# Optimization experiments

Measured on AMD Instinct MI355X. Metric: run time of the kernel, lower is better.

The kernel has to match this reference:

```python
import jax, jax.numpy as jnp
import numpy as np

N_NODES = 100000
N_EDGES = 500000
N_GRAPHS = 128
HID = 128          # Config.hidden_dim
KEY_EMB = HID // 4 # 32
IN_DIM = 16
FEAT_DIM = IN_DIM - 1  # key feature removed
OUT_DIM = 2
MSG_IN = 2 * HID + 1   # 257


def setup_inputs() -> dict:
    key = jax.random.key(0)
    ks = jax.random.split(key, 24)
    p = lambda k, shp: (jax.random.normal(k, shp, dtype=jnp.float32) * 0.02)
    inp = {
        "x": jax.random.normal(ks[0], (N_NODES, IN_DIM), dtype=jnp.float32),
        "W_enc": p(ks[1], (1, KEY_EMB)), "b_enc": jnp.zeros((KEY_EMB,), jnp.float32),
        "W0": p(ks[2], (FEAT_DIM + KEY_EMB, HID)), "b0": jnp.zeros((HID,), jnp.float32),
        "W1a": p(ks[3], (MSG_IN, HID)), "b1a": jnp.zeros((HID,), jnp.float32),
        "W1b": p(ks[4], (HID, HID)), "b1b": jnp.zeros((HID,), jnp.float32),
        "W2a": p(ks[5], (MSG_IN, HID)), "b2a": jnp.zeros((HID,), jnp.float32),
        "W2b": p(ks[6], (HID, HID)), "b2b": jnp.zeros((HID,), jnp.float32),
        "Wf1": p(ks[7], (4 * HID, HID)), "bf1": jnp.zeros((HID,), jnp.float32),
        "Wf2": p(ks[8], (HID, OUT_DIM)), "bf2": jnp.zeros((OUT_DIM,), jnp.float32),
        "edge_src1": jax.random.randint(ks[9], (N_EDGES,), 0, N_NODES),
        "edge_dst1": jax.random.randint(ks[10], (N_EDGES,), 0, N_NODES),
        "edge_src2": jax.random.randint(ks[11], (N_EDGES,), 0, N_NODES),
        "edge_dst2": jax.random.randint(ks[12], (N_EDGES,), 0, N_NODES),
        "batch": jnp.sort(jax.random.randint(ks[13], (N_NODES,), 0, N_GRAPHS)),
    }
    return inp


def _leaky_relu(v):
    return jnp.where(v > 0, v, 0.1 * v)


def _edge_conv(h, key_feat, src, dst, Wa, ba, Wb, bb):
    # message: [x_j - x_i, x_i, key_j - key_i] -> Linear -> LeakyReLU(0.1) -> Linear
    h_i = h[dst]                      # [E, HID] target
    h_j = h[src]                      # [E, HID] source
    m = jnp.concatenate([h_j - h_i, h_i, key_feat[src] - key_feat[dst]], axis=-1)  # [E, 257]
    m = _leaky_relu(jnp.dot(m, Wa) + ba)
    m = jnp.dot(m, Wb) + bb
    agg = jax.ops.segment_max(m, dst, num_segments=N_NODES)
    agg = jnp.where(jnp.isfinite(agg), agg, 0.0)  # nodes with no in-edges -> 0 (PyG scatter-max fill)
    return agg + h  # residual


def reference(x, W_enc, b_enc, W0, b0, W1a, b1a, W1b, b1b, W2a, b2a, W2b, b2b,
              Wf1, bf1, Wf2, bf2, edge_src1, edge_dst1, edge_src2, edge_dst2, batch):
    key_feat = x[:, 0:1]              # key_feature_idx = 0
    features = x[:, 1:]               # [N, FEAT_DIM]
    key_emb = jnp.dot(key_feat, W_enc) + b_enc  # [N, 32]
    h = jax.nn.relu(jnp.dot(jnp.concatenate([features, key_emb], axis=-1), W0) + b0)  # dropout: eval mode

    x1 = jax.nn.relu(_edge_conv(h, key_feat, edge_src1, edge_dst1, W1a, b1a, W1b, b1b))
    x2 = jax.nn.relu(_edge_conv(x1, key_feat, edge_src2, edge_dst2, W2a, b2a, W2b, b2b))

    cat = jnp.concatenate([x1, x2], axis=1)  # [N, 256]
    max_pool = jax.ops.segment_max(cat, batch, num_segments=N_GRAPHS)
    max_pool = jnp.where(jnp.isfinite(max_pool), max_pool, 0.0)
    counts = jax.ops.segment_sum(jnp.ones((N_NODES,), jnp.float32), batch, num_segments=N_GRAPHS)
    mean_pool = jax.ops.segment_sum(cat, batch, num_segments=N_GRAPHS) / jnp.maximum(counts, 1.0)[:, None]

    pooled = jnp.concatenate([max_pool, mean_pool], axis=1)  # [G, 512]
    out = jnp.dot(jax.nn.relu(jnp.dot(pooled, Wf1) + bf1), Wf2) + bf2
    return jax.nn.log_softmax(out, axis=1)
```

## Files before the change

### kernel.cpp

```cpp
#include <hip/hip_runtime.h>
#include <cstdint>

#define N_NODES 100000
#define N_EDGES 500000
#define N_GRAPHS 128
#define HID 128
#define SCAN1_B ((2 * N_NODES + 255) / 256)
#define BOTH_GRID ((2 * N_EDGES + 255) / 256)

typedef __attribute__((ext_vector_type(8))) short short8;
typedef __attribute__((ext_vector_type(4))) float f32x4;

__device__ __forceinline__ unsigned encf(float f) {
    unsigned u = __float_as_uint(f);
    return (u & 0x80000000u) ? ~u : (u | 0x80000000u);
}
__device__ __forceinline__ float decf(unsigned e) {
    unsigned u = (e & 0x80000000u) ? (e & 0x7FFFFFFFu) : ~e;
    return __uint_as_float(u);
}
__device__ __forceinline__ unsigned pk_bf16(float a, float b) {
    unsigned ua = __float_as_uint(a);
    unsigned ub = __float_as_uint(b);
    ua = (ua + 0x7fffu + ((ua >> 16) & 1u)) >> 16;
    ub = (ub + 0x7fffu + ((ub >> 16) & 1u)) & 0xffff0000u;
    return ua | ub;
}
__device__ __forceinline__ ushort bf16r(float f) {
    unsigned u = __float_as_uint(f);
    return (ushort)((u + 0x7fffu + ((u >> 16) & 1u)) >> 16);
}
__device__ __forceinline__ float bf2f(ushort h) {
    return __uint_as_float((unsigned)h << 16);
}

__global__ __launch_bounds__(256) void transp_prep_kernel(const float* __restrict__ W1b,
                                                          const float* __restrict__ W2b,
                                                          const float* __restrict__ W1a,
                                                          const float* __restrict__ W2a,
                                                          const float* __restrict__ W_enc,
                                                          const float* __restrict__ b_enc,
                                                          const float* __restrict__ W0,
                                                          const float* __restrict__ b0,
                                                          ushort* __restrict__ WT,
                                                          float* __restrict__ wkey,
                                                          float* __restrict__ bias0,
                                                          int* __restrict__ cnt,
                                                          float* __restrict__ pooled) {
    int blk = blockIdx.x;
    int tid = threadIdx.x;
    if (blk >= 385) {
        int z = blk - 385;
        if (z < SCAN1_B) {
            int i = z * 256 + tid;
            if (i < 2 * N_NODES) cnt[i] = 0;
        } else {
            int i = (z - SCAN1_B) * 256 + tid;
            pooled[i] = 0.f;
        }
        return;
    }
    if (blk == 384) {
        if (tid < HID) {
            float wk = 0.f, bk = b0[tid];
            for (int k = 0; k < 32; ++k) {
                float w = W0[(15 + k) * HID + tid];
                wk += W_enc[k] * w;
                bk += b_enc[k] * w;
            }
            wkey[tid] = wk;
            bias0[tid] = bk;
        }
        return;
    }
    int m = blk >> 6;
    int i = (blk & 63) * 256 + tid;
    int n = i >> 7, k = i & 127;
    int src = k * HID + n;
    float v;
    switch (m) {
        case 0: v = W1b[src]; break;
        case 1: v = W2b[src]; break;
        case 2: v = W1a[src]; break;
        case 3: v = W1a[HID * HID + src] - W1a[src]; break;
        case 4: v = W2a[src]; break;
        default: v = W2a[HID * HID + src] - W2a[src]; break;
    }
    WT[m * HID * HID + i] = bf16r(v);
}

__global__ __launch_bounds__(256) void encode_hist_kernel(const float* __restrict__ x,
                                                          const float* __restrict__ W0,
                                                          const float* __restrict__ wkey,
                                                          const float* __restrict__ bias0,
                                                          ushort* __restrict__ h,
                                                          float* __restrict__ xkey,
                                                          const int* __restrict__ dst1,
                                                          const int* __restrict__ dst2,
                                                          int* __restrict__ cnt,
                                                          int* __restrict__ seq) {
    int blk = blockIdx.x;
    int tid = threadIdx.x;
    if (blk < BOTH_GRID) {
        int e = blk * 256 + tid;
        if (e < N_EDGES) seq[e] = atomicAdd(&cnt[dst1[e]], 1);
        else if (e < 2 * N_EDGES) seq[e] = atomicAdd(&cnt[N_NODES + dst2[e - N_EDGES]], 1);
        return;
    }
    int nb = blk - BOTH_GRID;
    int n = nb * 2 + (tid >> 7);
    int j = tid & 127;
    const float* xr = x + n * 16;
    float k0 = xr[0];
    if (j == 0) xkey[n] = k0;
    float acc = bias0[j] + k0 * wkey[j];
#pragma unroll
    for (int f = 0; f < 15; ++f)
        acc = fmaf(xr[1 + f], W0[f * HID + j], acc);
    h[n * HID + j] = bf16r(fmaxf(acc, 0.f));
}

__global__ __launch_bounds__(512, 4) void mm_mfma_dual_kernel(const ushort* __restrict__ in,
                                                              const unsigned* __restrict__ aggin,
                                                              const int* __restrict__ cntin,
                                                              const float* __restrict__ baddin,
                                                              ushort* __restrict__ xout,
                                                              const ushort* __restrict__ WuT,
                                                              const ushort* __restrict__ WvT,
                                                              const float* __restrict__ bv,
                                                              ushort* __restrict__ outu,
                                                              ushort* __restrict__ outv, int nrows) {
    __shared__ ushort sH[128 * 136];
    __shared__ ushort sWT[128 * 136];
    int tid = threadIdx.x;
    int n0 = blockIdx.x * 128;
#pragma unroll
    for (int q = 0; q < 4; ++q) {
        int c = q * 512 + tid;
        int r = c >> 4, off = (c & 15) << 3;
        int n = n0 + r;
        uint4 vv = make_uint4(0, 0, 0, 0);
        if (n < nrows) {
            uint4 hv = *(const uint4*)(in + (size_t)n * HID + off);
            if (aggin) {
                float add[8];
#pragma unroll
                for (int p = 0; p < 8; ++p) add[p] = 0.f;
                if (cntin[n] > 0) {
                    uint4 e0 = *(const uint4*)(aggin + (size_t)n * HID + off);
                    uint4 e1 = *(const uint4*)(aggin + (size_t)n * HID + off + 4);
                    float4 bb0 = *(const float4*)(baddin + off);
                    float4 bb1 = *(const float4*)(baddin + off + 4);
                    add[0] = decf(e0.x) + bb0.x; add[1] = decf(e0.y) + bb0.y;
                    add[2] = decf(e0.z) + bb0.z; add[3] = decf(e0.w) + bb0.w;
                    add[4] = decf(e1.x) + bb1.x; add[5] = decf(e1.y) + bb1.y;
                    add[6] = decf(e1.z) + bb1.z; add[7] = decf(e1.w) + bb1.w;
                }
                unsigned hw[4] = {hv.x, hv.y, hv.z, hv.w};
                unsigned ow[4];
#pragma unroll
                for (int p = 0; p < 4; ++p) {
                    float lo = __uint_as_float(hw[p] << 16);
                    float hi = __uint_as_float(hw[p] & 0xffff0000u);
                    float r0 = fmaxf(add[2 * p] + lo, 0.f);
                    float r1 = fmaxf(add[2 * p + 1] + hi, 0.f);
                    ow[p] = pk_bf16(r0, r1);
                }
                vv = make_uint4(ow[0], ow[1], ow[2], ow[3]);
                *(uint4*)(xout + (size_t)n * HID + off) = vv;
            } else {
                vv = hv;
            }
        }
        *(uint4*)(sH + r * 136 + off) = vv;
    }
#pragma unroll
    for (int q = 0; q < 4; ++q) {
        int c = q * 512 + tid;
        int nn = c >> 4, off = (c & 15) << 3;
        *(uint4*)(sWT + nn * 136 + off) = *(const uint4*)(WuT + nn * 128 + off);
    }
    __syncthreads();

    int lane = tid & 63, wv = tid >> 6;
    int l15 = lane & 15, quad = lane >> 4;
    int ch = wv & 1, rh = wv >> 1;

    short8 afr[2][4];
#pragma unroll
    for (int rr = 0; rr < 2; ++rr) {
        const ushort* ab = sH + (rh * 32 + rr * 16 + l15) * 136 + quad * 8;
#pragma unroll
        for (int kc = 0; kc < 4; ++kc)
            afr[rr][kc] = *(const short8*)(ab + kc * 32);
    }

#pragma unroll
    for (int pass = 0; pass < 2; ++pass) {
        ushort* out = pass ? outv : outu;
        f32x4 acc[2][4];
#pragma unroll
        for (int rr = 0; rr < 2; ++rr)
#pragma unroll
            for (int ct = 0; ct < 4; ++ct) acc[rr][ct] = (f32x4){0.f, 0.f, 0.f, 0.f};
#pragma unroll
        for (int kc = 0; kc < 4; ++kc) {
#pragma unroll
            for (int ct = 0; ct < 4; ++ct) {
                short8 bfr = *(const short8*)(sWT + ((ch * 4 + ct) * 16 + l15) * 136 + quad * 8 + kc * 32);
                acc[0][ct] = __builtin_amdgcn_mfma_f32_16x16x32_bf16(afr[0][kc], bfr, acc[0][ct], 0, 0, 0);
                acc[1][ct] = __builtin_amdgcn_mfma_f32_16x16x32_bf16(afr[1][kc], bfr, acc[1][ct], 0, 0, 0);
            }
        }
        __syncthreads();
#pragma unroll
        for (int ct = 0; ct < 4; ++ct) {
            int col = (ch * 4 + ct) * 16 + l15;
            float bb = pass ? bv[col] : 0.f;
#pragma unroll
            for (int rr = 0; rr < 2; ++rr) {
                int rowb = rh * 32 + rr * 16 + quad * 4;
#pragma unroll
                for (int reg = 0; reg < 4; ++reg)
                    sH[(rowb + reg) * 136 + col] = bf16r(acc[rr][ct][reg] + bb);
            }
        }
        if (pass == 0) {
#pragma unroll
            for (int q = 0; q < 4; ++q) {
                int c = q * 512 + tid;
                int nn = c >> 4, off = (c & 15) << 3;
                *(uint4*)(sWT + nn * 136 + off) = *(const uint4*)(WvT + nn * 128 + off);
            }
        }
        __syncthreads();
#pragma unroll
        for (int q = 0; q < 4; ++q) {
            int c = q * 512 + tid;
            int r = c >> 4, off = (c & 15) << 3;
            int m = n0 + r;
            if (m < nrows)
                *(uint4*)(out + (size_t)m * HID + off) = *(const uint4*)(sH + r * 136 + off);
        }
    }
}

__global__ __launch_bounds__(256) void scan1_kernel(const int* __restrict__ cnt,
                                                    int* __restrict__ cursor,
                                                    int* __restrict__ partials) {
    __shared__ int tmp[256];
    int tid = threadIdx.x;
    int gid = blockIdx.x * 256 + tid;
    int v = (gid < 2 * N_NODES) ? cnt[gid] : 0;
    tmp[tid] = v;
    __syncthreads();
#pragma unroll
    for (int off = 1; off < 256; off <<= 1) {
        int t = (tid >= off) ? tmp[tid - off] : 0;
        __syncthreads();
        tmp[tid] += t;
        __syncthreads();
    }
    if (gid < 2 * N_NODES) cursor[gid] = tmp[tid] - v;
    if (tid == 255) partials[blockIdx.x] = tmp[255];
}

__global__ __launch_bounds__(1024) void scan2_kernel(int* __restrict__ partials) {
    __shared__ int tmp[1024];
    int tid = threadIdx.x;
    int v = (tid < SCAN1_B) ? partials[tid] : 0;
    tmp[tid] = v;
    __syncthreads();
#pragma unroll
    for (int off = 1; off < 1024; off <<= 1) {
        int t = (tid >= off) ? tmp[tid - off] : 0;
        __syncthreads();
        tmp[tid] += t;
        __syncthreads();
    }
    if (tid < SCAN1_B) partials[tid] = tmp[tid] - v;
}

__global__ __launch_bounds__(256) void build_kernel(const int* __restrict__ src1,
                                                    const int* __restrict__ dst1,
                                                    const int* __restrict__ src2,
                                                    const int* __restrict__ dst2,
                                                    const int* __restrict__ cnt,
                                                    const int* __restrict__ cursor,
                                                    const int* __restrict__ partials,
                                                    const int* __restrict__ seq,
                                                    int* __restrict__ srcS,
                                                    int* __restrict__ dstS,
                                                    unsigned* __restrict__ agg1,
                                                    unsigned* __restrict__ agg2) {
    int blk = blockIdx.x;
    int tid = threadIdx.x;
    if (blk < SCAN1_B) {
        int gid = blk * 256 + tid;
        if (gid >= 2 * N_NODES) return;
        int c = cnt[gid];
        if (c == 0) return;
        int o = cursor[gid] + partials[gid >> 8];
        int layer = gid >= N_NODES;
        int d = gid - layer * N_NODES;
        for (int i = 0; i < c; ++i) dstS[o + i] = d;
        bool spans = (o >> 4) != ((o + c - 1) >> 4);
        bool tail = (o + c == N_EDGES) || (o + c == 2 * N_EDGES);
        if (spans || tail) {
            unsigned* agg = layer ? agg2 : agg1;
            uint4* ap = (uint4*)(agg + (size_t)d * HID);
#pragma unroll
            for (int i = 0; i < 32; ++i) ap[i] = make_uint4(0u, 0u, 0u, 0u);
        }
        return;
    }
    int e = (blk - SCAN1_B) * 256 + tid;
    int s, idx;
    if (e < N_EDGES) { s = src1[e]; idx = dst1[e]; }
    else if (e < 2 * N_EDGES) { s = src2[e - N_EDGES]; idx = N_NODES + dst2[e - N_EDGES]; }
    else return;
    int pos = cursor[idx] + partials[idx >> 8] + seq[e];
    srcS[pos] = s;
}

__global__ __launch_bounds__(512, 6) void edge_kernel(const ushort* __restrict__ u,
                                                      const ushort* __restrict__ v,
                                                      const float* __restrict__ xkey,
                                                      const int* __restrict__ srcS,
                                                      const int* __restrict__ dstS,
                                                      const ushort* __restrict__ WbT,
                                                      const float* __restrict__ wlast,
                                                      unsigned* __restrict__ agg) {
    __shared__ ushort sWT[128 * 136];
    __shared__ ushort sU[64 * 136];
    __shared__ int sDst[64];
    __shared__ int sBnd[2];
    __shared__ unsigned sMask[3];
    int tid = threadIdx.x;
    int w0 = blockIdx.x * 64;

#pragma unroll
    for (int q = 0; q < 4; ++q) {
        int c = q * 512 + tid;
        int n = c >> 4, off = (c & 15) << 3;
        *(uint4*)(sWT + n * 136 + off) = *(const uint4*)(WbT + n * 128 + off);
    }

    int eloc = tid >> 3;
    int sub = tid & 7;
    int kb = sub << 4;
    int lane = tid & 63, wv = tid >> 6;
    int l15 = lane & 15, quad = lane >> 4;
    int ch = wv & 1, rh = wv >> 1;

    float wreg[16];
    {
        const float4* wr4 = (const float4*)(wlast + kb);
#pragma unroll
        for (int q = 0; q < 4; ++q) {
            float4 wq = wr4[q];
            wreg[q * 4 + 0] = wq.x; wreg[q * 4 + 1] = wq.y;
            wreg[q * 4 + 2] = wq.z; wreg[q * 4 + 3] = wq.w;
        }
    }

    {
        int e = w0 + eloc;
        if (e >= N_EDGES) e = N_EDGES - 1;
        int sx = srcS[e], sy = dstS[e];
        if (sub == 0) sDst[eloc] = sy;
        if (tid < 2) {
            int eb = (tid == 0) ? (w0 - 1) : (w0 + 64);
            sBnd[tid] = (eb >= 0 && eb < N_EDGES) ? dstS[eb] : -1;
        }
        float kd = xkey[sx] - xkey[sy];
        const uint4* ur = (const uint4*)(u + (size_t)sx * HID + kb);
        const uint4* vr = (const uint4*)(v + (size_t)sy * HID + kb);
        uint4 uu[2], vvv[2];
        uu[0] = ur[0]; uu[1] = ur[1];
        vvv[0] = vr[0]; vvv[1] = vr[1];
#pragma unroll
        for (int q = 0; q < 2; ++q) {
            unsigned pu[4] = {uu[q].x, uu[q].y, uu[q].z, uu[q].w};
            unsigned pv[4] = {vvv[q].x, vvv[q].y, vvv[q].z, vvv[q].w};
            unsigned pk[4];
#pragma unroll
            for (int p = 0; p < 4; ++p) {
                float a0 = __uint_as_float(pu[p] << 16) + __uint_as_float(pv[p] << 16);
                float a1 = __uint_as_float(pu[p] & 0xffff0000u) + __uint_as_float(pv[p] & 0xffff0000u);
                a0 = fmaf(kd, wreg[q * 8 + 2 * p], a0);
                a1 = fmaf(kd, wreg[q * 8 + 2 * p + 1], a1);
                a0 = fmaxf(a0, 0.1f * a0);
                a1 = fmaxf(a1, 0.1f * a1);
                pk[p] = pk_bf16(a0, a1);
            }
            uint4 o; o.x = pk[0]; o.y = pk[1]; o.z = pk[2]; o.w = pk[3];
            *(uint4*)(sU + eloc * 136 + kb + q * 8) = o;
        }
    }
    __syncthreads();

    if (tid < 64) {
        int dprev = (tid == 0) ? sBnd[0] : sDst[tid - 1];
        unsigned long long m = __ballot(sDst[tid] != dprev);
        if (tid == 0) { sMask[0] = (unsigned)m; sMask[1] = (unsigned)(m >> 32); }
        if (tid == 63) sMask[2] = (sDst[63] != sBnd[1]) ? 1u : 0u;
    }

    short8 afr[4];
    {
        const ushort* ab = sU + (rh * 16 + l15) * 136 + quad * 8;
#pragma unroll
        for (int kc = 0; kc < 4; ++kc)
            afr[kc] = *(const short8*)(ab + kc * 32);
    }
    f32x4 acc[4];
#pragma unroll
    for (int ct = 0; ct < 4; ++ct) acc[ct] = (f32x4){0.f, 0.f, 0.f, 0.f};
#pragma unroll
    for (int kc = 0; kc < 4; ++kc) {
#pragma unroll
        for (int ct = 0; ct < 4; ++ct) {
            short8 bfr = *(const short8*)(sWT + ((ch * 4 + ct) * 16 + l15) * 136 + quad * 8 + kc * 32);
            acc[ct] = __builtin_amdgcn_mfma_f32_16x16x32_bf16(afr[kc], bfr, acc[ct], 0, 0, 0);
        }
    }
    __syncthreads();

#pragma unroll
    for (int ct = 0; ct < 4; ++ct) {
        int col = (ch * 4 + ct) * 16 + l15;
        uint2 pr;
        pr.x = pk_bf16(acc[ct][0], acc[ct][1]);
        pr.y = pk_bf16(acc[ct][2], acc[ct][3]);
        *(uint2*)(sU + col * 66 + rh * 16 + quad * 4) = pr;
    }
    __syncthreads();

    {
        int j = tid & 127;
        int q4 = tid >> 7;
        int base = q4 * 16;
        const ushort* mrow = sU + j * 66 + base;
        float vals[16];
#pragma unroll
        for (int q = 0; q < 4; ++q) {
            ushort4 mv = *(const ushort4*)(mrow + q * 4);
            vals[q * 4 + 0] = bf2f(mv.x);
            vals[q * 4 + 1] = bf2f(mv.y);
            vals[q * 4 + 2] = bf2f(mv.z);
            vals[q * 4 + 3] = bf2f(mv.w);
        }
        unsigned mlo = __builtin_amdgcn_readfirstlane(sMask[0]);
        unsigned mhi = __builtin_amdgcn_readfirstlane(sMask[1]);
        unsigned b64 = __builtin_amdgcn_readfirstlane(sMask[2]);
        unsigned long long mask = ((unsigned long long)mhi << 32) | mlo;
        unsigned slice = (unsigned)((mask >> base) & 0xFFFFull);
        unsigned nextbit = (q4 == 3) ? (b64 & 1u) : (unsigned)((mask >> (base + 16)) & 1ull);
        unsigned ext = slice | (nextbit << 16);
        bool contFrom = !(ext & 1u);
        float run = 0.f;
        bool first = true;
#pragma unroll
        for (int e3 = 0; e3 < 16; ++e3) {
            float vv2 = vals[e3];
            bool hb = (ext >> e3) & 1u;
            run = (e3 == 0 || hb) ? vv2 : fmaxf(run, vv2);
            bool end = (e3 == 15) || ((ext >> (e3 + 1)) & 1u);
            if (end) {
                int d = sDst[base + e3];
                unsigned en = encf(run);
                unsigned* ap = agg + (size_t)d * HID + j;
                bool useAtomic = (first && contFrom) || ((e3 == 15) && !nextbit);
                if (useAtomic) atomicMax(ap, en);
                else *ap = en;
                first = false;
            }
        }
    }
}

__global__ __launch_bounds__(256) void pool_kernel(const ushort* __restrict__ x1,
                                                   const unsigned* __restrict__ agg2,
                                                   const float* __restrict__ b2b,
                                                   const int* __restrict__ cnt2,
                                                   const int* __restrict__ batch,
                                                   float* __restrict__ pooled) {
    int g = blockIdx.x >> 4, s = blockIdx.x & 15;
    int tid = threadIdx.x;
    int lo = 0, hi = N_NODES;
    while (lo < hi) { int mid = (lo + hi) >> 1; if (batch[mid] < g) lo = mid + 1; else hi = mid; }
    int start = lo;
    hi = N_NODES;
    while (lo < hi) { int mid = (lo + hi) >> 1; if (batch[mid] < g + 1) lo = mid + 1; else hi = mid; }
    int end = lo;
    int cnt = end - start;
    int b0 = start + (int)((long long)cnt * s / 16);
    int b1 = start + (int)((long long)cnt * (s + 1) / 16);
    if (b1 <= b0) return;
    int j = tid & 127;
    bool isx2 = tid >= 128;
    float bbj = isx2 ? b2b[j] : 0.f;
    float mx = -INFINITY, sm = 0.f;
    for (int n = b0; n < b1; ++n) {
        float xv = bf2f(x1[(size_t)n * HID + j]);
        float vv;
        if (isx2) {
            float a = 0.f;
            if (cnt2[n] > 0) a = decf(agg2[(size_t)n * HID + j]) + bbj;
            vv = fmaxf(a + xv, 0.f);
        } else {
            vv = xv;
        }
        mx = fmaxf(mx, vv);
        sm += vv;
    }
    atomicMax((unsigned*)pooled + (size_t)g * 512 + tid, encf(mx));
    atomicAdd(pooled + (size_t)g * 512 + 256 + tid, sm);
}

__global__ __launch_bounds__(128) void final_kernel(const float* __restrict__ pooled,
                                                    const int* __restrict__ batch,
                                                    const float* __restrict__ Wf1,
                                                    const float* __restrict__ bf1,
                                                    const float* __restrict__ Wf2,
                                                    const float* __restrict__ bf2,
                                                    float* __restrict__ out) {
    __shared__ float sP[512];
    __shared__ float sH[128];
    int g = blockIdx.x, tid = threadIdx.x;
    int lo = 0, hi = N_NODES;
    while (lo < hi) { int mid = (lo + hi) >> 1; if (batch[mid] < g) lo = mid + 1; else hi = mid; }
    int start = lo;
    hi = N_NODES;
    while (lo < hi) { int mid = (lo + hi) >> 1; if (batch[mid] < g + 1) lo = mid + 1; else hi = mid; }
    int cnt = lo - start;
    float inv = 1.f / (float)(cnt > 1 ? cnt : 1);
#pragma unroll
    for (int q = 0; q < 4; ++q) {
        int idx = q * 128 + tid;
        float raw;
        if (idx < 256) {
            unsigned e = ((const unsigned*)pooled)[(size_t)g * 512 + idx];
            raw = (e == 0u) ? 0.f : decf(e);
        } else {
            raw = pooled[(size_t)g * 512 + idx] * inv;
        }
        sP[idx] = raw;
    }
    __syncthreads();
    float acc = bf1[tid];
    for (int k = 0; k < 512; ++k) acc = fmaf(sP[k], Wf1[k * HID + tid], acc);
    sH[tid] = fmaxf(acc, 0.f);
    __syncthreads();
    if (tid < 2) {
        float l = bf2[tid];
        for (int k = 0; k < 128; ++k) l = fmaf(sH[k], Wf2[k * 2 + tid], l);
        sP[tid] = l;
    }
    __syncthreads();
    if (tid == 0) {
        float l0 = sP[0], l1 = sP[1];
        float m = fmaxf(l0, l1);
        float ls = m + logf(expf(l0 - m) + expf(l1 - m));
        out[g * 2 + 0] = l0 - ls;
        out[g * 2 + 1] = l1 - ls;
    }
}

extern "C" void kernel_launch(void* const* d_in, const int* in_sizes, int n_in,
                              void* d_out, int out_size, void* d_ws, size_t ws_size,
                              hipStream_t stream) {
    const float* x     = (const float*)d_in[0];
    const float* W_enc = (const float*)d_in[1];
    const float* b_enc = (const float*)d_in[2];
    const float* W0    = (const float*)d_in[3];
    const float* b0    = (const float*)d_in[4];
    const float* W1a   = (const float*)d_in[5];
    const float* b1a   = (const float*)d_in[6];
    const float* W1b   = (const float*)d_in[7];
    const float* b1b   = (const float*)d_in[8];
    const float* W2a   = (const float*)d_in[9];
    const float* b2a   = (const float*)d_in[10];
    const float* W2b   = (const float*)d_in[11];
    const float* b2b   = (const float*)d_in[12];
    const float* Wf1   = (const float*)d_in[13];
    const float* bf1   = (const float*)d_in[14];
    const float* Wf2   = (const float*)d_in[15];
    const float* bf2   = (const float*)d_in[16];
    const int* src1    = (const int*)d_in[17];
    const int* dst1    = (const int*)d_in[18];
    const int* src2    = (const int*)d_in[19];
    const int* dst2    = (const int*)d_in[20];
    const int* batch   = (const int*)d_in[21];

    const size_t NB = (size_t)N_NODES * HID;
    ushort* hbuf  = (ushort*)d_ws;
    unsigned* agg1 = (unsigned*)(hbuf + NB);
    unsigned* agg2 = agg1 + NB;
    ushort* ubuf  = (ushort*)(agg2 + NB);
    ushort* vbuf  = ubuf + NB;
    ushort* WT    = vbuf + NB;
    ushort* WbT1 = WT;
    ushort* WbT2 = WT + 1 * HID * HID;
    ushort* WuT1 = WT + 2 * HID * HID;
    ushort* WvT1 = WT + 3 * HID * HID;
    ushort* WuT2 = WT + 4 * HID * HID;
    ushort* WvT2 = WT + 5 * HID * HID;
    float* wkey  = (float*)(WT + 6 * HID * HID);
    float* bias0 = wkey + 128;
    float* xkey  = bias0 + 128;
    float* pooled = xkey + N_NODES;
    int* cnt    = (int*)(pooled + 128 * 512);
    int* cursor = cnt + 2 * N_NODES;
    int* partials = cursor + 2 * N_NODES;
    int* srcS = partials + 1024;
    int* dstS = srcS + 2 * N_EDGES;
    int* seq  = dstS + 2 * N_EDGES;

    const int edgeGrid = (N_EDGES + 63) / 64;
    const int mmGrid   = (N_NODES + 127) / 128;
    const int prepGrid = 385 + SCAN1_B + 256;
    const int encHistGrid = BOTH_GRID + N_NODES / 2;
    const int buildGrid = SCAN1_B + BOTH_GRID;

    transp_prep_kernel<<<prepGrid, 256, 0, stream>>>(W1b, W2b, W1a, W2a, W_enc, b_enc, W0, b0,
                                                     WT, wkey, bias0, cnt, pooled);
    encode_hist_kernel<<<encHistGrid, 256, 0, stream>>>(x, W0, wkey, bias0, hbuf, xkey,
                                                        dst1, dst2, cnt, seq);

    scan1_kernel<<<SCAN1_B, 256, 0, stream>>>(cnt, cursor, partials);
    scan2_kernel<<<1, 1024, 0, stream>>>(partials);
    build_kernel<<<buildGrid, 256, 0, stream>>>(src1, dst1, src2, dst2, cnt, cursor, partials,
                                                seq, srcS, dstS, agg1, agg2);

    mm_mfma_dual_kernel<<<mmGrid, 512, 0, stream>>>(hbuf, nullptr, nullptr, nullptr, nullptr,
                                                    WuT1, WvT1, b1a, ubuf, vbuf, N_NODES);
    edge_kernel<<<edgeGrid, 512, 0, stream>>>(ubuf, vbuf, xkey, srcS, dstS, WbT1,
                                              W1a + 256 * HID, agg1);

    mm_mfma_dual_kernel<<<mmGrid, 512, 0, stream>>>(hbuf, agg1, cnt, b1b, hbuf,
                                                    WuT2, WvT2, b2a, ubuf, vbuf, N_NODES);
    edge_kernel<<<edgeGrid, 512, 0, stream>>>(ubuf, vbuf, xkey, srcS + N_EDGES, dstS + N_EDGES,
                                              WbT2, W2a + 256 * HID, agg2);

    pool_kernel<<<N_GRAPHS * 16, 256, 0, stream>>>(hbuf, agg2, b2b, cnt + N_NODES, batch, pooled);
    final_kernel<<<N_GRAPHS, 128, 0, stream>>>(pooled, batch, Wf1, bf1, Wf2, bf2, (float*)d_out);
}
```

Measured before the change: 492.5 us.

## Fuse node encoding into first matmul and merge CSR build with it

The node encoder (x·W0 + key embedding, ReLU) now runs inside the first MFMA dual-matmul kernel. That kernel also carries the CSR build work (dst fill, agg zeroing, src scatter) as extra blocks, and the histogram moves into the prep kernel. The cnt buffer is zeroed with hipMemsetAsync instead of kernel blocks. This removes two launches and a round trip of h through memory before the first matmul, at the cost of a larger heterogeneous kernel whose build blocks share occupancy limits with the MFMA blocks.

New measurement: 463.3 us. 5.9% less time.

```diff
diff --git a/kernel.cpp b/kernel.cpp
--- a/kernel.cpp
+++ b/kernel.cpp
@@ -7,6 +7,9 @@
 #define HID 128
 #define SCAN1_B ((2 * N_NODES + 255) / 256)
 #define BOTH_GRID ((2 * N_EDGES + 255) / 256)
+#define MM_G ((N_NODES + 127) / 128)
+#define A_G ((2 * N_NODES + 511) / 512)
+#define B_G ((2 * N_EDGES + 511) / 512)
 
 typedef __attribute__((ext_vector_type(8))) short short8;
 typedef __attribute__((ext_vector_type(4))) float f32x4;
@@ -34,30 +37,32 @@
     return __uint_as_float((unsigned)h << 16);
 }
 
-__global__ __launch_bounds__(256) void transp_prep_kernel(const float* __restrict__ W1b,
-                                                          const float* __restrict__ W2b,
-                                                          const float* __restrict__ W1a,
-                                                          const float* __restrict__ W2a,
-                                                          const float* __restrict__ W_enc,
-                                                          const float* __restrict__ b_enc,
-                                                          const float* __restrict__ W0,
-                                                          const float* __restrict__ b0,
-                                                          ushort* __restrict__ WT,
-                                                          float* __restrict__ wkey,
-                                                          float* __restrict__ bias0,
-                                                          int* __restrict__ cnt,
-                                                          float* __restrict__ pooled) {
+__global__ __launch_bounds__(256) void prep_hist_kernel(const float* __restrict__ W1b,
+                                                        const float* __restrict__ W2b,
+                                                        const float* __restrict__ W1a,
+                                                        const float* __restrict__ W2a,
+                                                        const float* __restrict__ W_enc,
+                                                        const float* __restrict__ b_enc,
+                                                        const float* __restrict__ W0,
+                                                        const float* __restrict__ b0,
+                                                        ushort* __restrict__ WT,
+                                                        float* __restrict__ wkey,
+                                                        float* __restrict__ bias0,
+                                                        float* __restrict__ pooled,
+                                                        const int* __restrict__ dst1,
+                                                        const int* __restrict__ dst2,
+                                                        int* __restrict__ cnt,
+                                                        int* __restrict__ seq) {
     int blk = blockIdx.x;
     int tid = threadIdx.x;
+    if (blk >= 641) {
+        int e = (blk - 641) * 256 + tid;
+        if (e < N_EDGES) seq[e] = atomicAdd(&cnt[dst1[e]], 1);
+        else if (e < 2 * N_EDGES) seq[e] = atomicAdd(&cnt[N_NODES + dst2[e - N_EDGES]], 1);
+        return;
+    }
     if (blk >= 385) {
-        int z = blk - 385;
-        if (z < SCAN1_B) {
-            int i = z * 256 + tid;
-            if (i < 2 * N_NODES) cnt[i] = 0;
-        } else {
-            int i = (z - SCAN1_B) * 256 + tid;
-            pooled[i] = 0.f;
-        }
+        pooled[(blk - 385) * 256 + tid] = 0.f;
         return;
     }
     if (blk == 384) {
@@ -89,35 +94,203 @@
     WT[m * HID * HID + i] = bf16r(v);
 }
 
-__global__ __launch_bounds__(256) void encode_hist_kernel(const float* __restrict__ x,
+__global__ __launch_bounds__(256) void scan1_kernel(const int* __restrict__ cnt,
+                                                    int* __restrict__ cursor,
+                                                    int* __restrict__ partials) {
+    __shared__ int tmp[256];
+    int tid = threadIdx.x;
+    int gid = blockIdx.x * 256 + tid;
+    int v = (gid < 2 * N_NODES) ? cnt[gid] : 0;
+    tmp[tid] = v;
+    __syncthreads();
+#pragma unroll
+    for (int off = 1; off < 256; off <<= 1) {
+        int t = (tid >= off) ? tmp[tid - off] : 0;
+        __syncthreads();
+        tmp[tid] += t;
+        __syncthreads();
+    }
+    if (gid < 2 * N_NODES) cursor[gid] = tmp[tid] - v;
+    if (tid == 255) partials[blockIdx.x] = tmp[255];
+}
+
+__global__ __launch_bounds__(1024) void scan2_kernel(int* __restrict__ partials) {
+    __shared__ int tmp[1024];
+    int tid = threadIdx.x;
+    int v = (tid < SCAN1_B) ? partials[tid] : 0;
+    tmp[tid] = v;
+    __syncthreads();
+#pragma unroll
+    for (int off = 1; off < 1024; off <<= 1) {
+        int t = (tid >= off) ? tmp[tid - off] : 0;
+        __syncthreads();
+        tmp[tid] += t;
+        __syncthreads();
+    }
+    if (tid < SCAN1_B) partials[tid] = tmp[tid] - v;
+}
+
+__global__ __launch_bounds__(512, 4) void build_mm_kernel(const float* __restrict__ x,
                                                           const float* __restrict__ W0,
                                                           const float* __restrict__ wkey,
                                                           const float* __restrict__ bias0,
                                                           ushort* __restrict__ h,
                                                           float* __restrict__ xkey,
+                                                          const ushort* __restrict__ WuT,
+                                                          const ushort* __restrict__ WvT,
+                                                          const float* __restrict__ bv,
+                                                          ushort* __restrict__ outu,
+                                                          ushort* __restrict__ outv,
+                                                          const int* __restrict__ src1,
                                                           const int* __restrict__ dst1,
+                                                          const int* __restrict__ src2,
                                                           const int* __restrict__ dst2,
-                                                          int* __restrict__ cnt,
-                                                          int* __restrict__ seq) {
+                                                          const int* __restrict__ cnt,
+                                                          const int* __restrict__ cursor,
+                                                          const int* __restrict__ partials,
+                                                          const int* __restrict__ seq,
+                                                          int* __restrict__ srcS,
+                                                          int* __restrict__ dstS,
+                                                          unsigned* __restrict__ agg1,
+                                                          unsigned* __restrict__ agg2) {
+    __shared__ ushort sH[128 * 136];
+    __shared__ ushort sWT[128 * 136];
     int blk = blockIdx.x;
     int tid = threadIdx.x;
-    if (blk < BOTH_GRID) {
-        int e = blk * 256 + tid;
-        if (e < N_EDGES) seq[e] = atomicAdd(&cnt[dst1[e]], 1);
-        else if (e < 2 * N_EDGES) seq[e] = atomicAdd(&cnt[N_NODES + dst2[e - N_EDGES]], 1);
+
+    if (blk >= MM_G) {
+        int zb = blk - MM_G;
+        if (zb < A_G) {
+            int gid = zb * 512 + tid;
+            if (gid >= 2 * N_NODES) return;
+            int c = cnt[gid];
+            if (c == 0) return;
+            int o = cursor[gid] + partials[gid >> 8];
+            int layer = gid >= N_NODES;
+            int d = gid - layer * N_NODES;
+            for (int i = 0; i < c; ++i) dstS[o + i] = d;
+            bool spans = (o >> 4) != ((o + c - 1) >> 4);
+            bool tail = (o + c == N_EDGES) || (o + c == 2 * N_EDGES);
+            if (spans || tail) {
+                unsigned* agg = layer ? agg2 : agg1;
+                uint4* ap = (uint4*)(agg + (size_t)d * HID);
+#pragma unroll
+                for (int i = 0; i < 32; ++i) ap[i] = make_uint4(0u, 0u, 0u, 0u);
+            }
+            return;
+        }
+        int e = (zb - A_G) * 512 + tid;
+        int s, idx;
+        if (e < N_EDGES) { s = src1[e]; idx = dst1[e]; }
+        else if (e < 2 * N_EDGES) { s = src2[e - N_EDGES]; idx = N_NODES + dst2[e - N_EDGES]; }
+        else return;
+        int pos = cursor[idx] + partials[idx >> 8] + seq[e];
+        srcS[pos] = s;
         return;
     }
-    int nb = blk - BOTH_GRID;
-    int n = nb * 2 + (tid >> 7);
-    int j = tid & 127;
-    const float* xr = x + n * 16;
-    float k0 = xr[0];
-    if (j == 0) xkey[n] = k0;
-    float acc = bias0[j] + k0 * wkey[j];
-#pragma unroll
-    for (int f = 0; f < 15; ++f)
-        acc = fmaf(xr[1 + f], W0[f * HID + j], acc);
-    h[n * HID + j] = bf16r(fmaxf(acc, 0.f));
+
+    int n0 = blk * 128;
+#pragma unroll
+    for (int q = 0; q < 4; ++q) {
+        int c = q * 512 + tid;
+        int r = c >> 4, off = (c & 15) << 3;
+        int n = n0 + r;
+        uint4 vv = make_uint4(0, 0, 0, 0);
+        if (n < N_NODES) {
+            const float* xr = x + n * 16;
+            float k0 = xr[0];
+            if (off == 0) xkey[n] = k0;
+            float xf[15];
+#pragma unroll
+            for (int f = 0; f < 15; ++f) xf[f] = xr[1 + f];
+            unsigned ow[4];
+#pragma unroll
+            for (int p = 0; p < 4; ++p) {
+                int c0 = off + 2 * p;
+                float a0 = bias0[c0] + k0 * wkey[c0];
+                float a1 = bias0[c0 + 1] + k0 * wkey[c0 + 1];
+#pragma unroll
+                for (int f = 0; f < 15; ++f) {
+                    float2 w2 = *(const float2*)(W0 + f * HID + c0);
+                    a0 = fmaf(xf[f], w2.x, a0);
+                    a1 = fmaf(xf[f], w2.y, a1);
+                }
+                ow[p] = pk_bf16(fmaxf(a0, 0.f), fmaxf(a1, 0.f));
+            }
+            vv = make_uint4(ow[0], ow[1], ow[2], ow[3]);
+            *(uint4*)(h + (size_t)n * HID + off) = vv;
+        }
+        *(uint4*)(sH + r * 136 + off) = vv;
+    }
+#pragma unroll
+    for (int q = 0; q < 4; ++q) {
+        int c = q * 512 + tid;
+        int nn = c >> 4, off = (c & 15) << 3;
+        *(uint4*)(sWT + nn * 136 + off) = *(const uint4*)(WuT + nn * 128 + off);
+    }
+    __syncthreads();
+
+    int lane = tid & 63, wv = tid >> 6;
+    int l15 = lane & 15, quad = lane >> 4;
+    int ch = wv & 1, rh = wv >> 1;
+
+    short8 afr[2][4];
+#pragma unroll
+    for (int rr = 0; rr < 2; ++rr) {
+        const ushort* ab = sH + (rh * 32 + rr * 16 + l15) * 136 + quad * 8;
+#pragma unroll
+        for (int kc = 0; kc < 4; ++kc)
+            afr[rr][kc] = *(const short8*)(ab + kc * 32);
+    }
+
+#pragma unroll
+    for (int pass = 0; pass < 2; ++pass) {
+        ushort* out = pass ? outv : outu;
+        f32x4 acc[2][4];
+#pragma unroll
+        for (int rr = 0; rr < 2; ++rr)
+#pragma unroll
+            for (int ct = 0; ct < 4; ++ct) acc[rr][ct] = (f32x4){0.f, 0.f, 0.f, 0.f};
+#pragma unroll
+        for (int kc = 0; kc < 4; ++kc) {
+#pragma unroll
+            for (int ct = 0; ct < 4; ++ct) {
+                short8 bfr = *(const short8*)(sWT + ((ch * 4 + ct) * 16 + l15) * 136 + quad * 8 + kc * 32);
+                acc[0][ct] = __builtin_amdgcn_mfma_f32_16x16x32_bf16(afr[0][kc], bfr, acc[0][ct], 0, 0, 0);
+                acc[1][ct] = __builtin_amdgcn_mfma_f32_16x16x32_bf16(afr[1][kc], bfr, acc[1][ct], 0, 0, 0);
+            }
+        }
+        __syncthreads();
+#pragma unroll
+        for (int ct = 0; ct < 4; ++ct) {
+            int col = (ch * 4 + ct) * 16 + l15;
+            float bb = pass ? bv[col] : 0.f;
+#pragma unroll
+            for (int rr = 0; rr < 2; ++rr) {
+                int rowb = rh * 32 + rr * 16 + quad * 4;
+#pragma unroll
+                for (int reg = 0; reg < 4; ++reg)
+                    sH[(rowb + reg) * 136 + col] = bf16r(acc[rr][ct][reg] + bb);
+            }
+        }
+        if (pass == 0) {
+#pragma unroll
+            for (int q = 0; q < 4; ++q) {
+                int c = q * 512 + tid;
+                int nn = c >> 4, off = (c & 15) << 3;
+                *(uint4*)(sWT + nn * 136 + off) = *(const uint4*)(WvT + nn * 128 + off);
+            }
+        }
+        __syncthreads();
+#pragma unroll
+        for (int q = 0; q < 4; ++q) {
+            int c = q * 512 + tid;
+            int r = c >> 4, off = (c & 15) << 3;
+            int m = n0 + r;
+            if (m < N_NODES)
+                *(uint4*)(out + (size_t)m * HID + off) = *(const uint4*)(sH + r * 136 + off);
+        }
+    }
 }
 
 __global__ __launch_bounds__(512, 4) void mm_mfma_dual_kernel(const ushort* __restrict__ in,
@@ -142,35 +315,31 @@
         uint4 vv = make_uint4(0, 0, 0, 0);
         if (n < nrows) {
             uint4 hv = *(const uint4*)(in + (size_t)n * HID + off);
-            if (aggin) {
-                float add[8];
-#pragma unroll
-                for (int p = 0; p < 8; ++p) add[p] = 0.f;
-                if (cntin[n] > 0) {
-                    uint4 e0 = *(const uint4*)(aggin + (size_t)n * HID + off);
-                    uint4 e1 = *(const uint4*)(aggin + (size_t)n * HID + off + 4);
-                    float4 bb0 = *(const float4*)(baddin + off);
-                    float4 bb1 = *(const float4*)(baddin + off + 4);
-                    add[0] = decf(e0.x) + bb0.x; add[1] = decf(e0.y) + bb0.y;
-                    add[2] = decf(e0.z) + bb0.z; add[3] = decf(e0.w) + bb0.w;
-                    add[4] = decf(e1.x) + bb1.x; add[5] = decf(e1.y) + bb1.y;
-                    add[6] = decf(e1.z) + bb1.z; add[7] = decf(e1.w) + bb1.w;
-                }
-                unsigned hw[4] = {hv.x, hv.y, hv.z, hv.w};
-                unsigned ow[4];
-#pragma unroll
-                for (int p = 0; p < 4; ++p) {
-                    float lo = __uint_as_float(hw[p] << 16);
-                    float hi = __uint_as_float(hw[p] & 0xffff0000u);
-                    float r0 = fmaxf(add[2 * p] + lo, 0.f);
-                    float r1 = fmaxf(add[2 * p + 1] + hi, 0.f);
-                    ow[p] = pk_bf16(r0, r1);
-                }
-                vv = make_uint4(ow[0], ow[1], ow[2], ow[3]);
-                *(uint4*)(xout + (size_t)n * HID + off) = vv;
-            } else {
-                vv = hv;
-            }
+            float add[8];
+#pragma unroll
+            for (int p = 0; p < 8; ++p) add[p] = 0.f;
+            if (cntin[n] > 0) {
+                uint4 e0 = *(const uint4*)(aggin + (size_t)n * HID + off);
+                uint4 e1 = *(const uint4*)(aggin + (size_t)n * HID + off + 4);
+                float4 bb0 = *(const float4*)(baddin + off);
+                float4 bb1 = *(const float4*)(baddin + off + 4);
+                add[0] = decf(e0.x) + bb0.x; add[1] = decf(e0.y) + bb0.y;
+                add[2] = decf(e0.z) + bb0.z; add[3] = decf(e0.w) + bb0.w;
+                add[4] = decf(e1.x) + bb1.x; add[5] = decf(e1.y) + bb1.y;
+                add[6] = decf(e1.z) + bb1.z; add[7] = decf(e1.w) + bb1.w;
+            }
+            unsigned hw[4] = {hv.x, hv.y, hv.z, hv.w};
+            unsigned ow[4];
+#pragma unroll
+            for (int p = 0; p < 4; ++p) {
+                float lo = __uint_as_float(hw[p] << 16);
+                float hi = __uint_as_float(hw[p] & 0xffff0000u);
+                float r0 = fmaxf(add[2 * p] + lo, 0.f);
+                float r1 = fmaxf(add[2 * p + 1] + hi, 0.f);
+                ow[p] = pk_bf16(r0, r1);
+            }
+            vv = make_uint4(ow[0], ow[1], ow[2], ow[3]);
+            *(uint4*)(xout + (size_t)n * HID + off) = vv;
         }
         *(uint4*)(sH + r * 136 + off) = vv;
     }
@@ -243,84 +412,6 @@
                 *(uint4*)(out + (size_t)m * HID + off) = *(const uint4*)(sH + r * 136 + off);
         }
     }
-}
-
-__global__ __launch_bounds__(256) void scan1_kernel(const int* __restrict__ cnt,
-                                                    int* __restrict__ cursor,
-                                                    int* __restrict__ partials) {
-    __shared__ int tmp[256];
-    int tid = threadIdx.x;
-    int gid = blockIdx.x * 256 + tid;
-    int v = (gid < 2 * N_NODES) ? cnt[gid] : 0;
-    tmp[tid] = v;
-    __syncthreads();
-#pragma unroll
-    for (int off = 1; off < 256; off <<= 1) {
-        int t = (tid >= off) ? tmp[tid - off] : 0;
-        __syncthreads();
-        tmp[tid] += t;
-        __syncthreads();
-    }
-    if (gid < 2 * N_NODES) cursor[gid] = tmp[tid] - v;
-    if (tid == 255) partials[blockIdx.x] = tmp[255];
-}
-
-__global__ __launch_bounds__(1024) void scan2_kernel(int* __restrict__ partials) {
-    __shared__ int tmp[1024];
-    int tid = threadIdx.x;
-    int v = (tid < SCAN1_B) ? partials[tid] : 0;
-    tmp[tid] = v;
-    __syncthreads();
-#pragma unroll
-    for (int off = 1; off < 1024; off <<= 1) {
-        int t = (tid >= off) ? tmp[tid - off] : 0;
-        __syncthreads();
-        tmp[tid] += t;
-        __syncthreads();
-    }
-    if (tid < SCAN1_B) partials[tid] = tmp[tid] - v;
-}
-
-__global__ __launch_bounds__(256) void build_kernel(const int* __restrict__ src1,
-                                                    const int* __restrict__ dst1,
-                                                    const int* __restrict__ src2,
-                                                    const int* __restrict__ dst2,
-                                                    const int* __restrict__ cnt,
-                                                    const int* __restrict__ cursor,
-                                                    const int* __restrict__ partials,
-                                                    const int* __restrict__ seq,
-                                                    int* __restrict__ srcS,
-                                                    int* __restrict__ dstS,
-                                                    unsigned* __restrict__ agg1,
-                                                    unsigned* __restrict__ agg2) {
-    int blk = blockIdx.x;
-    int tid = threadIdx.x;
-    if (blk < SCAN1_B) {
-        int gid = blk * 256 + tid;
-        if (gid >= 2 * N_NODES) return;
-        int c = cnt[gid];
-        if (c == 0) return;
-        int o = cursor[gid] + partials[gid >> 8];
-        int layer = gid >= N_NODES;
-        int d = gid - layer * N_NODES;
-        for (int i = 0; i < c; ++i) dstS[o + i] = d;
-        bool spans = (o >> 4) != ((o + c - 1) >> 4);
-        bool tail = (o + c == N_EDGES) || (o + c == 2 * N_EDGES);
-        if (spans || tail) {
-            unsigned* agg = layer ? agg2 : agg1;
-            uint4* ap = (uint4*)(agg + (size_t)d * HID);
-#pragma unroll
-            for (int i = 0; i < 32; ++i) ap[i] = make_uint4(0u, 0u, 0u, 0u);
-        }
-        return;
-    }
-    int e = (blk - SCAN1_B) * 256 + tid;
-    int s, idx;
-    if (e < N_EDGES) { s = src1[e]; idx = dst1[e]; }
-    else if (e < 2 * N_EDGES) { s = src2[e - N_EDGES]; idx = N_NODES + dst2[e - N_EDGES]; }
-    else return;
-    int pos = cursor[idx] + partials[idx >> 8] + seq[e];
-    srcS[pos] = s;
 }
 
 __global__ __launch_bounds__(512, 6) void edge_kernel(const ushort* __restrict__ u,
@@ -619,28 +710,25 @@
     int* seq  = dstS + 2 * N_EDGES;
 
     const int edgeGrid = (N_EDGES + 63) / 64;
-    const int mmGrid   = (N_NODES + 127) / 128;
-    const int prepGrid = 385 + SCAN1_B + 256;
-    const int encHistGrid = BOTH_GRID + N_NODES / 2;
-    const int buildGrid = SCAN1_B + BOTH_GRID;
-
-    transp_prep_kernel<<<prepGrid, 256, 0, stream>>>(W1b, W2b, W1a, W2a, W_enc, b_enc, W0, b0,
-                                                     WT, wkey, bias0, cnt, pooled);
-    encode_hist_kernel<<<encHistGrid, 256, 0, stream>>>(x, W0, wkey, bias0, hbuf, xkey,
-                                                        dst1, dst2, cnt, seq);
-
+    const int prepGrid = 385 + 256 + BOTH_GRID;
+    const int buildMmGrid = MM_G + A_G + B_G;
+
+    hipMemsetAsync(cnt, 0, 2 * N_NODES * sizeof(int), stream);
+    prep_hist_kernel<<<prepGrid, 256, 0, stream>>>(W1b, W2b, W1a, W2a, W_enc, b_enc, W0, b0,
+                                                   WT, wkey, bias0, pooled, dst1, dst2, cnt, seq);
     scan1_kernel<<<SCAN1_B, 256, 0, stream>>>(cnt, cursor, partials);
     scan2_kernel<<<1, 1024, 0, stream>>>(partials);
-    build_kernel<<<buildGrid, 256, 0, stream>>>(src1, dst1, src2, dst2, cnt, cursor, partials,
-                                                seq, srcS, dstS, agg1, agg2);
-
-    mm_mfma_dual_kernel<<<mmGrid, 512, 0, stream>>>(hbuf, nullptr, nullptr, nullptr, nullptr,
-                                                    WuT1, WvT1, b1a, ubuf, vbuf, N_NODES);
+
+    build_mm_kernel<<<buildMmGrid, 512, 0, stream>>>(x, W0, wkey, bias0, hbuf, xkey,
+                                                     WuT1, WvT1, b1a, ubuf, vbuf,
+                                                     src1, dst1, src2, dst2, cnt, cursor,
+                                                     partials, seq, srcS, dstS, agg1, agg2);
+
     edge_kernel<<<edgeGrid, 512, 0, stream>>>(ubuf, vbuf, xkey, srcS, dstS, WbT1,
                                               W1a + 256 * HID, agg1);
 
-    mm_mfma_dual_kernel<<<mmGrid, 512, 0, stream>>>(hbuf, agg1, cnt, b1b, hbuf,
-                                                    WuT2, WvT2, b2a, ubuf, vbuf, N_NODES);
+    mm_mfma_dual_kernel<<<MM_G, 512, 0, stream>>>(hbuf, agg1, cnt, b1b, hbuf,
+                                                  WuT2, WvT2, b2a, ubuf, vbuf, N_NODES);
     edge_kernel<<<edgeGrid, 512, 0, stream>>>(ubuf, vbuf, xkey, srcS + N_EDGES, dstS + N_EDGES,
                                               WbT2, W2a + 256 * HID, agg2);
 
```
